# Kernel tuning notes

Measured on AMD Instinct MI355X. Metric: run time of the kernel, lower is better.

## Reference

```python
import jax, jax.numpy as jnp
import numpy as np

B_SZ, SEQ, D_MODEL = 2, 512, 1024
EXPAND, HEAD_DIM = 2, 64
D_INNER = EXPAND * D_MODEL            # 2048
N_HEADS = D_INNER // HEAD_DIM         # 32
D_STATE = 64
EPS = 1e-6
PROJ_DIM = 2 * D_INNER + 2 * N_HEADS * D_STATE + N_HEADS  # 8224


def setup_inputs() -> dict:
    key = jax.random.key(0)
    k = jax.random.split(key, 5)
    return {
        "hidden": jax.random.normal(k[0], (B_SZ, SEQ, D_MODEL), jnp.float32),
        "W_in": 0.02 * jax.random.normal(k[1], (D_MODEL, PROJ_DIM), jnp.float32),
        "dt_bias": 0.5 * jax.random.normal(k[2], (N_HEADS,), jnp.float32),
        "A_log": 0.5 * jax.random.normal(k[3], (N_HEADS,), jnp.float32),
        "norm_weight": jnp.ones((D_INNER,), jnp.float32),
        "W_out": 0.02 * jax.random.normal(k[4], (D_INNER, D_MODEL), jnp.float32),
    }


def _rope(x, theta):
    # x: [b,l,h,n] interleaved pairs (view_as_complex convention); theta: [b,l,h,n//2]
    x0, x1 = x[..., 0::2], x[..., 1::2]
    c, s = jnp.cos(theta), jnp.sin(theta)
    y = jnp.stack([x0 * c - x1 * s, x0 * s + x1 * c], axis=-1)
    return y.reshape(x.shape)


def reference(hidden, W_in, dt_bias, A_log, norm_weight, W_out):
    b, l, _ = hidden.shape
    proj = hidden @ W_in  # [b,l,PROJ_DIM]
    hn = N_HEADS * D_STATE
    z = proj[..., :D_INNER]
    xr = proj[..., D_INNER:2 * D_INNER].reshape(b, l, N_HEADS, HEAD_DIM)
    Bm = proj[..., 2 * D_INNER:2 * D_INNER + hn].reshape(b, l, N_HEADS, D_STATE)
    Cm = proj[..., 2 * D_INNER + hn:2 * D_INNER + 2 * hn].reshape(b, l, N_HEADS, D_STATE)
    dt = jax.nn.softplus(proj[..., -N_HEADS:] + dt_bias)  # [b,l,h]

    A = -jnp.exp(A_log)                 # [h], negative decay
    alpha = jnp.exp(dt * A)             # decay factor
    beta = 0.5 * dt * alpha             # trapezoidal: half-step on previous input
    gamma = 0.5 * dt                    # trapezoidal: half-step on current input

    # data-dependent RoPE: phase is cumulative dt scaled by per-dim inverse freq
    half = D_STATE // 2
    inv_freq = 1.0 / (10000.0 ** (jnp.arange(half, dtype=jnp.float32) / half))
    theta = jnp.cumsum(dt, axis=1)[..., None] * inv_freq  # [b,l,h,half]
    Bm = _rope(Bm, theta)
    Cm = _rope(Cm, theta)

    # shifted (t-1) inputs, zero at t=0 (h starts at 0 so alpha-at-t0 is a no-op)
    Bp = jnp.pad(Bm[:, :-1], ((0, 0), (1, 0), (0, 0), (0, 0)))
    xp = jnp.pad(xr[:, :-1], ((0, 0), (1, 0), (0, 0), (0, 0)))

    tl = lambda t: jnp.moveaxis(t, 1, 0)  # time-major for scan
    xs = (tl(xr), tl(Bm), tl(Cm), tl(Bp), tl(xp), tl(alpha), tl(beta), tl(gamma))
    h0 = jnp.zeros((b, N_HEADS, D_STATE, HEAD_DIM), hidden.dtype)

    def step(h, inp):
        x_t, B_t, C_t, Bprev, xprev, a, bt, g = inp
        h = (a[..., None, None] * h
             + bt[..., None, None] * jnp.einsum('bhn,bhp->bhnp', Bprev, xprev)
             + g[..., None, None] * jnp.einsum('bhn,bhp->bhnp', B_t, x_t))
        y = jnp.einsum('bhn,bhnp->bhp', C_t, h)
        return h, y

    _, ys = jax.lax.scan(step, h0, xs)          # ys: [l,b,h,p]
    y = jnp.moveaxis(ys, 0, 1).reshape(b, l, D_INNER)

    y = y * jax.nn.silu(z)                      # gated output
    rms = jnp.sqrt(jnp.mean(y * y, axis=-1, keepdims=True) + EPS)
    y = y / rms * norm_weight                   # RMSNorm
    return y @ W_out
```

## Files before the change

kernel.cpp:

```cpp
#include <hip/hip_runtime.h>
#include <stdint.h>

typedef __attribute__((ext_vector_type(8))) short short8;
typedef __attribute__((ext_vector_type(8))) unsigned short ushort8;
typedef __attribute__((ext_vector_type(4))) unsigned short usv4;
typedef __attribute__((ext_vector_type(4))) float float4v;

#define B_SZ 2
#define SEQ 512
#define D_MODEL 1024
#define D_INNER 2048
#define N_HEADS 32
#define HEAD_DIM 64
#define D_STATE 64
#define PROJ_DIM 8224
#define NPAD 8320
#define MROWS 1024

__device__ __forceinline__ unsigned short f2bf(float f) {
    unsigned u = __builtin_bit_cast(unsigned, f);
    u += 0x7fffu + ((u >> 16) & 1u);
    return (unsigned short)(u >> 16);
}
__device__ __forceinline__ float bf2f(unsigned short h) {
    return __builtin_bit_cast(float, (unsigned)h << 16);
}

__device__ __forceinline__ void gld16(unsigned short* lds, const unsigned short* g) {
#if __has_builtin(__builtin_amdgcn_global_load_lds)
    __builtin_amdgcn_global_load_lds(
        (const __attribute__((address_space(1))) void*)g,
        (__attribute__((address_space(3))) void*)lds, 16, 0, 0);
#else
    *(short8*)lds = *(const short8*)g;
#endif
}

__device__ void transpose_body(const float* __restrict__ src,
                               unsigned short* __restrict__ dst,
                               int R, int C, int bx, int by, float* T, int tid) {
    int c0 = bx * 64, r0 = by * 64;
    int row = tid >> 2, cg = (tid & 3) * 16;
    #pragma unroll
    for (int k = 0; k < 4; k++) {
        int col = cg + k * 4;
        float4v v;
        if (c0 + col + 3 < C) {
            v = *(const float4v*)&src[(size_t)(r0 + row) * C + c0 + col];
        } else {
            #pragma unroll
            for (int e = 0; e < 4; e++)
                v[e] = (c0 + col + e < C) ? src[(size_t)(r0 + row) * C + c0 + col + e] : 0.f;
        }
        *(float4v*)&T[row * 68 + col] = v;
    }
    __syncthreads();
    int drow = tid >> 2, sg = (tid & 3) * 16;
    ushort8 v[2];
    #pragma unroll
    for (int k = 0; k < 16; k++) v[k >> 3][k & 7] = f2bf(T[(sg + k) * 68 + drow]);
    unsigned short* d = &dst[(size_t)(c0 + drow) * R + r0 + sg];
    *(ushort8*)&d[0] = v[0];
    *(ushort8*)&d[8] = v[1];
}

__global__ __launch_bounds__(256) void prep_fat(
    const float* __restrict__ hidden, const float* __restrict__ W_in,
    const float* __restrict__ W_out, unsigned short* __restrict__ Hb,
    unsigned short* __restrict__ Wt1, unsigned short* __restrict__ Wt2) {
    __shared__ float T[64 * 68];
    int blk = blockIdx.x, tid = threadIdx.x;
    if (blk < 1024) {
        int i = blk * 1024 + tid * 4;
        float4v v = *(const float4v*)&hidden[i];
        usv4 o;
        #pragma unroll
        for (int k = 0; k < 4; k++) o[k] = f2bf(v[k]);
        *(usv4*)&Hb[i] = o;
    } else if (blk < 3104) {
        int q = blk - 1024;
        transpose_body(W_in, Wt1, D_MODEL, PROJ_DIM, q % 130, q / 130, T, tid);
    } else {
        int q = blk - 3104;
        transpose_body(W_out, Wt2, D_INNER, D_MODEL, q % 16, q / 16, T, tid);
    }
}

template <bool BF16OUT>
__global__ __launch_bounds__(256) void gemm_bt(
    const unsigned short* __restrict__ A, const unsigned short* __restrict__ Bt,
    void* __restrict__ Cout, int M, int N, int K, int klen) {
    __shared__ unsigned short As[8192];
    __shared__ unsigned short Bs[8192];
    int tid = threadIdx.x;
    int lane = tid & 63, w = tid >> 6, quad = lane >> 4, l15 = lane & 15;
    int m0 = blockIdx.y * 128, n0 = blockIdx.x * 128;
    int kb = blockIdx.z * klen, ke = kb + klen;
    int wm = (w & 1) * 64, wn = (w >> 1) * 64;
    float4v acc[4][4];
    #pragma unroll
    for (int i = 0; i < 4; i++)
        #pragma unroll
        for (int j = 0; j < 4; j++) acc[i][j] = (float4v){0.f, 0.f, 0.f, 0.f};

    int rs = tid >> 3;
    int gl = ((tid & 7) ^ (rs & 7)) * 8;
    const unsigned short* ap = &A [(size_t)(m0 + rs) * K + gl];
    const unsigned short* bp = &Bt[(size_t)(n0 + rs) * K + gl];
    int rx = l15 & 7;

    for (int k0 = kb; k0 < ke; k0 += 64) {
        __syncthreads();
        #pragma unroll
        for (int p = 0; p < 4; p++) {
            gld16(&As[p * 2048 + tid * 8], ap + (size_t)(p * 32) * K + k0);
            gld16(&Bs[p * 2048 + tid * 8], bp + (size_t)(p * 32) * K + k0);
        }
        __syncthreads();
        #pragma unroll
        for (int kq = 0; kq < 2; kq++) {
            short8 af[4], bfr[4];
            #pragma unroll
            for (int mt = 0; mt < 4; mt++)
                af[mt] = *(const short8*)&As[(wm + mt * 16 + l15) * 64 + (((kq << 2) + quad) ^ rx) * 8];
            #pragma unroll
            for (int nt = 0; nt < 4; nt++)
                bfr[nt] = *(const short8*)&Bs[(wn + nt * 16 + l15) * 64 + (((kq << 2) + quad) ^ rx) * 8];
            #pragma unroll
            for (int mt = 0; mt < 4; mt++)
                #pragma unroll
                for (int nt = 0; nt < 4; nt++)
                    acc[mt][nt] = __builtin_amdgcn_mfma_f32_16x16x32_bf16(
                        af[mt], bfr[nt], acc[mt][nt], 0, 0, 0);
        }
    }
    #pragma unroll
    for (int mt = 0; mt < 4; mt++)
        #pragma unroll
        for (int nt = 0; nt < 4; nt++)
            #pragma unroll
            for (int r = 0; r < 4; r++) {
                int row = m0 + wm + mt * 16 + quad * 4 + r;
                int col = n0 + wn + nt * 16 + l15;
                if (col < N) {
                    if (BF16OUT)
                        ((unsigned short*)Cout)[(size_t)blockIdx.z * M * N + (size_t)row * N + col]
                            = f2bf(acc[mt][nt][r]);
                    else
                        ((float*)Cout)[(size_t)blockIdx.z * M * N + (size_t)row * N + col]
                            = acc[mt][nt][r];
                }
            }
}

__global__ __launch_bounds__(256) void reduce4(
    const float* __restrict__ P, float* __restrict__ out, int n) {
    int i = (blockIdx.x * 256 + threadIdx.x) * 4;
    float4v s = *(const float4v*)&P[i];
    #pragma unroll
    for (int z = 1; z < 4; z++) {
        float4v v = *(const float4v*)&P[(size_t)z * n + i];
        #pragma unroll
        for (int k = 0; k < 4; k++) s[k] += v[k];
    }
    *(float4v*)&out[i] = s;
}

__global__ __launch_bounds__(256) void dt_scan(
    const unsigned short* __restrict__ proj, const float* __restrict__ dt_bias,
    float* __restrict__ dt_arr, float* __restrict__ cum_arr) {
    __shared__ float chs[8];
    int bh = blockIdx.x;
    int b = bh >> 5, h = bh & 31;
    int tid = threadIdx.x, lane = tid & 63, w = tid >> 6;
    float bias = dt_bias[h];
    int t0 = w * 64 + lane, t1 = 256 + w * 64 + lane;
    float raw0 = bf2f(proj[(size_t)(b * SEQ + t0) * PROJ_DIM + 8192 + h]) + bias;
    float raw1 = bf2f(proj[(size_t)(b * SEQ + t1) * PROJ_DIM + 8192 + h]) + bias;
    float dt0 = raw0 > 20.f ? raw0 : log1pf(expf(raw0));
    float dt1 = raw1 > 20.f ? raw1 : log1pf(expf(raw1));
    float v0 = dt0, v1 = dt1;
    #pragma unroll
    for (int d = 1; d < 64; d <<= 1) {
        float n0 = __shfl_up(v0, d, 64);
        float n1 = __shfl_up(v1, d, 64);
        if (lane >= d) { v0 += n0; v1 += n1; }
    }
    if (lane == 63) { chs[w] = v0; chs[4 + w] = v1; }
    __syncthreads();
    float off0 = 0.f, off1 = 0.f;
    #pragma unroll
    for (int c = 0; c < 8; c++) {
        float s = chs[c];
        if (c < w) off0 += s;
        if (c < 4 + w) off1 += s;
    }
    dt_arr[bh * SEQ + t0] = dt0;  cum_arr[bh * SEQ + t0] = off0 + v0;
    dt_arr[bh * SEQ + t1] = dt1;  cum_arr[bh * SEQ + t1] = off1 + v1;
}

__global__ __launch_bounds__(256) void pack_fat(
    const unsigned short* __restrict__ proj, const float* __restrict__ cum_arr,
    unsigned short* __restrict__ Bh, unsigned short* __restrict__ Ch,
    unsigned short* __restrict__ Xt) {
    __shared__ unsigned short XT[64 * 72];
    int blk = blockIdx.x, tid = threadIdx.x;
    if (blk < 1024) {
        int m = blk, b = m >> 9, t = m & 511;
        const float k_l2 = 13.287712379549449f / 32.f;
        #pragma unroll
        for (int i = 0; i < 4; i++) {
            int q = i * 256 + tid;
            int h = q >> 5, j = q & 31;
            float cum = cum_arr[(b * 32 + h) * SEQ + t];
            float th = cum * exp2f(-(float)j * k_l2);
            float s, c;
            __sincosf(th, &s, &c);
            size_t rb = (size_t)m * PROJ_DIM;
            unsigned bu = *(const unsigned*)&proj[rb + 4096 + h * 64 + 2 * j];
            unsigned cu = *(const unsigned*)&proj[rb + 6144 + h * 64 + 2 * j];
            float b0 = bf2f((unsigned short)(bu & 0xffff)), b1 = bf2f((unsigned short)(bu >> 16));
            float c0 = bf2f((unsigned short)(cu & 0xffff)), c1 = bf2f((unsigned short)(cu >> 16));
            size_t dst = ((size_t)(b * 32 + h) * SEQ + t) * 64 + 2 * j;
            unsigned ob = (unsigned)f2bf(b0 * c - b1 * s) | ((unsigned)f2bf(b0 * s + b1 * c) << 16);
            unsigned oc = (unsigned)f2bf(c0 * c - c1 * s) | ((unsigned)f2bf(c0 * s + c1 * c) << 16);
            *(unsigned*)&Bh[dst] = ob;
            *(unsigned*)&Ch[dst] = oc;
        }
    } else {
        int q = blk - 1024;
        int bh = q >> 3, s0 = (q & 7) * 64;
        int b = bh >> 5, h = bh & 31;
        int r = tid >> 2, cg = (tid & 3) * 16;
        const unsigned short* src = &proj[(size_t)(b * SEQ + s0 + r) * PROJ_DIM + 2048 + h * 64 + cg];
        *(ushort8*)&XT[r * 72 + cg]     = *(const ushort8*)&src[0];
        *(ushort8*)&XT[r * 72 + cg + 8] = *(const ushort8*)&src[8];
        __syncthreads();
        int p = tid >> 2, sg = (tid & 3) * 16;
        ushort8 v[2];
        #pragma unroll
        for (int k = 0; k < 16; k++) v[k >> 3][k & 7] = XT[(sg + k) * 72 + p];
        unsigned short* dst = &Xt[((size_t)bh * 64 + p) * SEQ + s0 + sg];
        *(ushort8*)&dst[0] = v[0];
        *(ushort8*)&dst[8] = v[1];
    }
}

__global__ __launch_bounds__(256) void attn_scan(
    const unsigned short* __restrict__ Bh, const unsigned short* __restrict__ Ch,
    const unsigned short* __restrict__ Xt, const float* __restrict__ dt_arr,
    const float* __restrict__ cum_arr, const float* __restrict__ A_log,
    float* __restrict__ y_ws) {
    __shared__ unsigned short Bs[4096];
    __shared__ unsigned short Xs[4096];
    __shared__ unsigned short Ps[4096];
    int qt = blockIdx.x, bh = blockIdx.y;
    int b = bh >> 5, h = bh & 31;
    float Aneg = -expf(A_log[h]);
    int tid = threadIdx.x, lane = tid & 63, w = tid >> 6;
    int quad = lane >> 4, l15 = lane & 15;

    int qrow = qt * 64 + w * 16 + l15;
    const unsigned short* Cptr = Ch + ((size_t)bh * SEQ + qrow) * 64;
    short8 cf[2];
    cf[0] = *(const short8*)&Cptr[quad * 8];
    cf[1] = *(const short8*)&Cptr[32 + quad * 8];

    int trow[4];
    float cumt[4];
    #pragma unroll
    for (int r = 0; r < 4; r++) {
        trow[r] = qt * 64 + w * 16 + quad * 4 + r;
        cumt[r] = cum_arr[bh * SEQ + trow[r]];
    }
    float4v yacc[4];
    #pragma unroll
    for (int i = 0; i < 4; i++) yacc[i] = (float4v){0.f, 0.f, 0.f, 0.f};

    for (int st = 0; st <= qt; st++) {
        __syncthreads();
        const unsigned short* bsrc = Bh + ((size_t)bh * SEQ + st * 64) * 64;
        gld16(&Bs[tid * 8],         bsrc + tid * 8);
        gld16(&Bs[(tid + 256) * 8], bsrc + (tid + 256) * 8);
        const unsigned short* xsrc = Xt + (size_t)bh * 64 * SEQ + st * 64;
        {
            int e = tid;
            int p = e >> 3, so = (e & 7) * 8;
            gld16(&Xs[p * 64 + so], xsrc + (size_t)p * SEQ + so);
            e = tid + 256;
            p = e >> 3; so = (e & 7) * 8;
            gld16(&Xs[p * 64 + so], xsrc + (size_t)p * SEQ + so);
        }
        __syncthreads();
        float4v sacc[4];
        #pragma unroll
        for (int i = 0; i < 4; i++) sacc[i] = (float4v){0.f, 0.f, 0.f, 0.f};
        #pragma unroll
        for (int kk = 0; kk < 2; kk++)
            #pragma unroll
            for (int nt = 0; nt < 4; nt++) {
                short8 bf8 = *(const short8*)&Bs[(nt * 16 + l15) * 64 + kk * 32 + quad * 8];
                sacc[nt] = __builtin_amdgcn_mfma_f32_16x16x32_bf16(cf[kk], bf8, sacc[nt], 0, 0, 0);
            }
        #pragma unroll
        for (int nt = 0; nt < 4; nt++) {
            int s = st * 64 + nt * 16 + l15;
            float cums = cum_arr[bh * SEQ + s];
            float dts = dt_arr[bh * SEQ + s];
            float dts1 = (s + 1 < SEQ) ? dt_arr[bh * SEQ + s + 1] : 0.f;
            #pragma unroll
            for (int r = 0; r < 4; r++) {
                int t = trow[r];
                float wgt = (s > t) ? 0.f
                          : expf(Aneg * (cumt[r] - cums)) * 0.5f * (dts + ((s < t) ? dts1 : 0.f));
                Ps[w * 1024 + (quad * 4 + r) * 64 + nt * 16 + l15] = f2bf(sacc[nt][r] * wgt);
            }
        }
        __syncthreads();
        #pragma unroll
        for (int kk = 0; kk < 2; kk++) {
            short8 af = *(const short8*)&Ps[w * 1024 + l15 * 64 + kk * 32 + quad * 8];
            #pragma unroll
            for (int pt = 0; pt < 4; pt++) {
                short8 xf = *(const short8*)&Xs[(pt * 16 + l15) * 64 + kk * 32 + quad * 8];
                yacc[pt] = __builtin_amdgcn_mfma_f32_16x16x32_bf16(af, xf, yacc[pt], 0, 0, 0);
            }
        }
    }
    #pragma unroll
    for (int pt = 0; pt < 4; pt++)
        #pragma unroll
        for (int r = 0; r < 4; r++) {
            int t = trow[r];
            int p = pt * 16 + l15;
            y_ws[((size_t)b * SEQ + t) * D_INNER + h * 64 + p] = yacc[pt][r];
        }
}

__global__ __launch_bounds__(256) void gated_rmsnorm(
    const float* __restrict__ y_ws, const unsigned short* __restrict__ proj,
    const float* __restrict__ nw, unsigned short* __restrict__ Y2) {
    __shared__ float red[4];
    int m = blockIdx.x, tid = threadIdx.x;
    const float* yrow = y_ws + (size_t)m * D_INNER;
    const unsigned short* zrow = proj + (size_t)m * PROJ_DIM;
    int j0 = tid * 8;
    ushort8 zv = *(const ushort8*)&zrow[j0];
    float v[8];
    float ss = 0.f;
    #pragma unroll
    for (int k = 0; k < 8; k++) {
        float y = yrow[j0 + k];
        float z = bf2f(zv[k]);
        float g = y * (z / (1.f + expf(-z)));
        v[k] = g;
        ss += g * g;
    }
    #pragma unroll
    for (int d = 32; d > 0; d >>= 1) ss += __shfl_down(ss, d, 64);
    if ((tid & 63) == 0) red[tid >> 6] = ss;
    __syncthreads();
    float tot = red[0] + red[1] + red[2] + red[3];
    float inv = 1.0f / sqrtf(tot / (float)D_INNER + 1e-6f);
    #pragma unroll
    for (int k = 0; k < 8; k++)
        Y2[(size_t)m * D_INNER + j0 + k] = f2bf(v[k] * inv * nw[j0 + k]);
}


extern "C" void kernel_launch(void* const* d_in, const int* in_sizes, int n_in,
                              void* d_out, int out_size, void* d_ws, size_t ws_size,
                              hipStream_t stream) {
    const float* hidden   = (const float*)d_in[0];
    const float* W_in     = (const float*)d_in[1];
    const float* dt_bias  = (const float*)d_in[2];
    const float* A_log    = (const float*)d_in[3];
    const float* norm_w   = (const float*)d_in[4];
    const float* W_out    = (const float*)d_in[5];
    float* out = (float*)d_out;

    char* ws = (char*)d_ws;
    unsigned short* Wt1  = (unsigned short*)(ws);
    unsigned short* Hb   = (unsigned short*)(ws + 17039360);
    unsigned short* proj = (unsigned short*)(ws + 19136512);
    float* dt_arr        = (float*)(ws + 35979264);
    float* cum_arr       = (float*)(ws + 36110336);
    unsigned short* Bh   = (unsigned short*)(ws + 36241408);
    unsigned short* Ch   = (unsigned short*)(ws + 40435712);
    unsigned short* Xt   = (unsigned short*)(ws + 44630016);
    float* y_ws          = (float*)(ws + 48824320);
    unsigned short* Y2   = (unsigned short*)(ws + 57212928);
    unsigned short* Wt2  = (unsigned short*)(ws + 61407232);
    float* Pk = (float*)proj;

    prep_fat<<<3616, 256, 0, stream>>>(hidden, W_in, W_out, Hb, Wt1, Wt2);
    gemm_bt<true><<<dim3(NPAD / 128, MROWS / 128, 1), 256, 0, stream>>>(
        Hb, Wt1, proj, MROWS, PROJ_DIM, D_MODEL, D_MODEL);
    dt_scan<<<64, 256, 0, stream>>>(proj, dt_bias, dt_arr, cum_arr);
    pack_fat<<<1536, 256, 0, stream>>>(proj, cum_arr, Bh, Ch, Xt);
    attn_scan<<<dim3(8, 64), 256, 0, stream>>>(Bh, Ch, Xt, dt_arr, cum_arr, A_log, y_ws);
    gated_rmsnorm<<<MROWS, 256, 0, stream>>>(y_ws, proj, norm_w, Y2);
    gemm_bt<false><<<dim3(D_MODEL / 128, MROWS / 128, 4), 256, 0, stream>>>(
        Y2, Wt2, Pk, MROWS, D_MODEL, D_INNER, D_INNER / 4);
    reduce4<<<MROWS * D_MODEL / 1024, 256, 0, stream>>>(Pk, out, MROWS * D_MODEL);
}
```

Before: 192.1 us.

## Split causal attention scan into per-tile blocks with atomic accumulation

Each (query tile, source tile) pair of the causal chunked scan becomes its own workgroup, giving 36 blocks per head instead of 8 sequential-loop blocks. Partial outputs are combined with float atomic adds into y_ws, which the pack kernel now zeroes using extra blocks. LDS tiles are also XOR-swizzled to reduce bank conflicts. The trade is more parallelism and shorter per-block critical paths against extra atomic traffic, a zeroing pass, repeated C/cum loads per tile, and nondeterministic summation order.

```diff
diff --git a/kernel.cpp b/kernel.cpp
--- a/kernel.cpp
+++ b/kernel.cpp
@@ -202,7 +202,7 @@
 __global__ __launch_bounds__(256) void pack_fat(
     const unsigned short* __restrict__ proj, const float* __restrict__ cum_arr,
     unsigned short* __restrict__ Bh, unsigned short* __restrict__ Ch,
-    unsigned short* __restrict__ Xt) {
+    unsigned short* __restrict__ Xt, float* __restrict__ y_ws) {
     __shared__ unsigned short XT[64 * 72];
     int blk = blockIdx.x, tid = threadIdx.x;
     if (blk < 1024) {
@@ -227,7 +227,7 @@
             *(unsigned*)&Bh[dst] = ob;
             *(unsigned*)&Ch[dst] = oc;
         }
-    } else {
+    } else if (blk < 1536) {
         int q = blk - 1024;
         int bh = q >> 3, s0 = (q & 7) * 64;
         int b = bh >> 5, h = bh & 31;
@@ -243,10 +243,13 @@
         unsigned short* dst = &Xt[((size_t)bh * 64 + p) * SEQ + s0 + sg];
         *(ushort8*)&dst[0] = v[0];
         *(ushort8*)&dst[8] = v[1];
-    }
-}
-
-__global__ __launch_bounds__(256) void attn_scan(
+    } else {
+        int q = blk - 1536;
+        *(float4v*)&y_ws[(size_t)q * 1024 + tid * 4] = (float4v){0.f, 0.f, 0.f, 0.f};
+    }
+}
+
+__global__ __launch_bounds__(256) void attn_tile(
     const unsigned short* __restrict__ Bh, const unsigned short* __restrict__ Ch,
     const unsigned short* __restrict__ Xt, const float* __restrict__ dt_arr,
     const float* __restrict__ cum_arr, const float* __restrict__ A_log,
@@ -254,11 +257,27 @@
     __shared__ unsigned short Bs[4096];
     __shared__ unsigned short Xs[4096];
     __shared__ unsigned short Ps[4096];
-    int qt = blockIdx.x, bh = blockIdx.y;
+    int pid = blockIdx.x;
+    int qt = 0, base = 0;
+    while (base + qt + 1 <= pid) { base += qt + 1; qt++; }
+    int st = pid - base;
+    int bh = blockIdx.y;
     int b = bh >> 5, h = bh & 31;
     float Aneg = -expf(A_log[h]);
     int tid = threadIdx.x, lane = tid & 63, w = tid >> 6;
     int quad = lane >> 4, l15 = lane & 15;
+    int rx = l15 & 7;
+
+    {
+        int srow = tid >> 3, sg = tid & 7;
+        int srow2 = srow + 32;
+        const unsigned short* bsrc = Bh + ((size_t)bh * SEQ + st * 64) * 64;
+        gld16(&Bs[tid * 8],         bsrc + srow * 64  + ((sg ^ (srow & 7)) * 8));
+        gld16(&Bs[(tid + 256) * 8], bsrc + srow2 * 64 + ((sg ^ (srow2 & 7)) * 8));
+        const unsigned short* xsrc = Xt + (size_t)bh * 64 * SEQ + st * 64;
+        gld16(&Xs[tid * 8],         xsrc + (size_t)srow * SEQ  + ((sg ^ (srow & 7)) * 8));
+        gld16(&Xs[(tid + 256) * 8], xsrc + (size_t)srow2 * SEQ + ((sg ^ (srow2 & 7)) * 8));
+    }
 
     int qrow = qt * 64 + w * 16 + l15;
     const unsigned short* Cptr = Ch + ((size_t)bh * SEQ + qrow) * 64;
@@ -273,58 +292,46 @@
         trow[r] = qt * 64 + w * 16 + quad * 4 + r;
         cumt[r] = cum_arr[bh * SEQ + trow[r]];
     }
+
+    __syncthreads();
+
+    float4v sacc[4];
+    #pragma unroll
+    for (int i = 0; i < 4; i++) sacc[i] = (float4v){0.f, 0.f, 0.f, 0.f};
+    #pragma unroll
+    for (int kk = 0; kk < 2; kk++)
+        #pragma unroll
+        for (int nt = 0; nt < 4; nt++) {
+            short8 bf8 = *(const short8*)&Bs[(nt * 16 + l15) * 64 + (((kk << 2) + quad) ^ rx) * 8];
+            sacc[nt] = __builtin_amdgcn_mfma_f32_16x16x32_bf16(cf[kk], bf8, sacc[nt], 0, 0, 0);
+        }
+    #pragma unroll
+    for (int nt = 0; nt < 4; nt++) {
+        int s = st * 64 + nt * 16 + l15;
+        float cums = cum_arr[bh * SEQ + s];
+        float dts = dt_arr[bh * SEQ + s];
+        float dts1 = (s + 1 < SEQ) ? dt_arr[bh * SEQ + s + 1] : 0.f;
+        #pragma unroll
+        for (int r = 0; r < 4; r++) {
+            int t = trow[r];
+            float wgt = (s > t) ? 0.f
+                      : expf(Aneg * (cumt[r] - cums)) * 0.5f * (dts + ((s < t) ? dts1 : 0.f));
+            int row = quad * 4 + r;
+            int col = nt * 16 + l15;
+            Ps[w * 1024 + row * 64 + (((col >> 3) ^ (row & 7)) << 3) + (col & 7)]
+                = f2bf(sacc[nt][r] * wgt);
+        }
+    }
     float4v yacc[4];
     #pragma unroll
     for (int i = 0; i < 4; i++) yacc[i] = (float4v){0.f, 0.f, 0.f, 0.f};
-
-    for (int st = 0; st <= qt; st++) {
-        __syncthreads();
-        const unsigned short* bsrc = Bh + ((size_t)bh * SEQ + st * 64) * 64;
-        gld16(&Bs[tid * 8],         bsrc + tid * 8);
-        gld16(&Bs[(tid + 256) * 8], bsrc + (tid + 256) * 8);
-        const unsigned short* xsrc = Xt + (size_t)bh * 64 * SEQ + st * 64;
-        {
-            int e = tid;
-            int p = e >> 3, so = (e & 7) * 8;
-            gld16(&Xs[p * 64 + so], xsrc + (size_t)p * SEQ + so);
-            e = tid + 256;
-            p = e >> 3; so = (e & 7) * 8;
-            gld16(&Xs[p * 64 + so], xsrc + (size_t)p * SEQ + so);
-        }
-        __syncthreads();
-        float4v sacc[4];
-        #pragma unroll
-        for (int i = 0; i < 4; i++) sacc[i] = (float4v){0.f, 0.f, 0.f, 0.f};
-        #pragma unroll
-        for (int kk = 0; kk < 2; kk++)
-            #pragma unroll
-            for (int nt = 0; nt < 4; nt++) {
-                short8 bf8 = *(const short8*)&Bs[(nt * 16 + l15) * 64 + kk * 32 + quad * 8];
-                sacc[nt] = __builtin_amdgcn_mfma_f32_16x16x32_bf16(cf[kk], bf8, sacc[nt], 0, 0, 0);
-            }
-        #pragma unroll
-        for (int nt = 0; nt < 4; nt++) {
-            int s = st * 64 + nt * 16 + l15;
-            float cums = cum_arr[bh * SEQ + s];
-            float dts = dt_arr[bh * SEQ + s];
-            float dts1 = (s + 1 < SEQ) ? dt_arr[bh * SEQ + s + 1] : 0.f;
-            #pragma unroll
-            for (int r = 0; r < 4; r++) {
-                int t = trow[r];
-                float wgt = (s > t) ? 0.f
-                          : expf(Aneg * (cumt[r] - cums)) * 0.5f * (dts + ((s < t) ? dts1 : 0.f));
-                Ps[w * 1024 + (quad * 4 + r) * 64 + nt * 16 + l15] = f2bf(sacc[nt][r] * wgt);
-            }
-        }
-        __syncthreads();
-        #pragma unroll
-        for (int kk = 0; kk < 2; kk++) {
-            short8 af = *(const short8*)&Ps[w * 1024 + l15 * 64 + kk * 32 + quad * 8];
-            #pragma unroll
-            for (int pt = 0; pt < 4; pt++) {
-                short8 xf = *(const short8*)&Xs[(pt * 16 + l15) * 64 + kk * 32 + quad * 8];
-                yacc[pt] = __builtin_amdgcn_mfma_f32_16x16x32_bf16(af, xf, yacc[pt], 0, 0, 0);
-            }
+    #pragma unroll
+    for (int kk = 0; kk < 2; kk++) {
+        short8 af = *(const short8*)&Ps[w * 1024 + l15 * 64 + (((kk << 2) + quad) ^ rx) * 8];
+        #pragma unroll
+        for (int pt = 0; pt < 4; pt++) {
+            short8 xf = *(const short8*)&Xs[(pt * 16 + l15) * 64 + (((kk << 2) + quad) ^ rx) * 8];
+            yacc[pt] = __builtin_amdgcn_mfma_f32_16x16x32_bf16(af, xf, yacc[pt], 0, 0, 0);
         }
     }
     #pragma unroll
@@ -333,7 +340,7 @@
         for (int r = 0; r < 4; r++) {
             int t = trow[r];
             int p = pt * 16 + l15;
-            y_ws[((size_t)b * SEQ + t) * D_INNER + h * 64 + p] = yacc[pt][r];
+            unsafeAtomicAdd(&y_ws[((size_t)b * SEQ + t) * D_INNER + h * 64 + p], yacc[pt][r]);
         }
 }
 
@@ -397,8 +404,8 @@
     gemm_bt<true><<<dim3(NPAD / 128, MROWS / 128, 1), 256, 0, stream>>>(
         Hb, Wt1, proj, MROWS, PROJ_DIM, D_MODEL, D_MODEL);
     dt_scan<<<64, 256, 0, stream>>>(proj, dt_bias, dt_arr, cum_arr);
-    pack_fat<<<1536, 256, 0, stream>>>(proj, cum_arr, Bh, Ch, Xt);
-    attn_scan<<<dim3(8, 64), 256, 0, stream>>>(Bh, Ch, Xt, dt_arr, cum_arr, A_log, y_ws);
+    pack_fat<<<3584, 256, 0, stream>>>(proj, cum_arr, Bh, Ch, Xt, y_ws);
+    attn_tile<<<dim3(36, 64), 256, 0, stream>>>(Bh, Ch, Xt, dt_arr, cum_arr, A_log, y_ws);
     gated_rmsnorm<<<MROWS, 256, 0, stream>>>(y_ws, proj, norm_w, Y2);
     gemm_bt<false><<<dim3(D_MODEL / 128, MROWS / 128, 4), 256, 0, stream>>>(
         Y2, Wt2, Pk, MROWS, D_MODEL, D_INNER, D_INNER / 4);
```

Result: slower. 198.5 us (+3.4%).
